# Kernel optimization log

Hardware: AMD Instinct MI355X
Metric: run time of the kernel (lower is better)

The kernel has to match this reference:

```python
import jax, jax.numpy as jnp
import numpy as np

B, M, P, A, T = 32, 128, 20, 32, 32
H = 32   # embed_size / local hidden
E = 64   # local_hidden_dim = 2*H, global attention embed dim


def setup_inputs() -> dict:
    key = jax.random.key(0)
    ks = jax.random.split(key, 10)
    def w(k, shape, fan):
        return jax.random.normal(k, shape, jnp.float32) / np.float32(np.sqrt(fan))
    z = lambda *s: jnp.zeros(s, jnp.float32)
    o = lambda *s: jnp.ones(s, jnp.float32)
    return {
        "map_states": jax.random.normal(ks[0], (B, M, P, 16), jnp.float32),
        "agent_states": jax.random.normal(ks[1], (B, A, T, 4), jnp.float32),
        "m_W1": w(ks[2], (16, H), 16), "m_b1": z(H), "m_g1": o(H), "m_be1": z(H),
        "m_W2": w(ks[3], (H, H), H),   "m_b2": z(H), "m_g2": o(H), "m_be2": z(H),
        "a_W1": w(ks[4], (4, H), 4),   "a_b1": z(H), "a_g1": o(H), "a_be1": z(H),
        "a_W2": w(ks[5], (H, H), H),   "a_b2": z(H), "a_g2": o(H), "a_be2": z(H),
        # stacked attention params: index 0 = a2m, 1 = agent(self), 2 = m2a
        "att_Wq": w(ks[6], (3, E, E), E), "att_bq": z(3, E),
        "att_Wk": w(ks[7], (3, E, E), E), "att_bk": z(3, E),
        "att_Wv": w(ks[8], (3, E, E), E), "att_bv": z(3, E),
        "att_Wo": w(ks[9], (3, E, E), E), "att_bo": z(3, E),
    }


def _mlp(x, W, b, g, be):
    # Linear -> LayerNorm -> ReLU
    h = x @ W + b
    mu = jnp.mean(h, axis=-1, keepdims=True)
    var = jnp.var(h, axis=-1, keepdims=True)
    h = (h - mu) / jnp.sqrt(var + 1e-5) * g + be
    return jax.nn.relu(h)


def _local_graph(x, p1, p2):
    # x: [B, N, P, F] -> [B, N, 2H]
    e = _mlp(_mlp(x, *p1), *p2)                       # [B,N,P,H]
    n = e.shape[2]
    # faithful "max excluding self": max_j (e[j] - 10000*[j==i])
    mask = -10000.0 * jnp.eye(n, dtype=e.dtype)       # [Pi,Pj]
    nb = jnp.max(e[:, :, None, :, :] + mask[None, None, :, :, None], axis=3)  # [B,N,P,H]
    e = jnp.concatenate([e, nb], axis=-1)             # [B,N,P,2H]
    return jnp.max(e, axis=2)                          # [B,N,2H]


def _mha(q, k, v, Wq, bq, Wk, bk, Wv, bv, Wo, bo):
    # single-head attention, batch_first
    d = q.shape[-1]
    Q = q @ Wq + bq
    K = k @ Wk + bk
    V = v @ Wv + bv
    scores = jnp.einsum('bqd,bkd->bqk', Q, K) / jnp.sqrt(jnp.asarray(d, Q.dtype))
    attn = jax.nn.softmax(scores, axis=-1)
    return jnp.einsum('bqk,bkd->bqd', attn, V) @ Wo + bo


def reference(map_states, agent_states,
              m_W1, m_b1, m_g1, m_be1, m_W2, m_b2, m_g2, m_be2,
              a_W1, a_b1, a_g1, a_be1, a_W2, a_b2, a_g2, a_be2,
              att_Wq, att_bq, att_Wk, att_bk, att_Wv, att_bv, att_Wo, att_bo):
    map_emb = _local_graph(map_states, (m_W1, m_b1, m_g1, m_be1), (m_W2, m_b2, m_g2, m_be2))      # [B,M,E]
    agent_emb = _local_graph(agent_states, (a_W1, a_b1, a_g1, a_be1), (a_W2, a_b2, a_g2, a_be2))  # [B,A,E]

    target = agent_emb[:, :1]                                       # [B,1,E]
    kv = jnp.concatenate([target, map_emb], axis=1)                 # [B,M+1,E]
    a2m = _mha(map_emb, kv, kv, att_Wq[0], att_bq[0], att_Wk[0], att_bk[0],
               att_Wv[0], att_bv[0], att_Wo[0], att_bo[0])
    map_emb = map_emb + a2m
    t_a = _mha(target, target, target, att_Wq[1], att_bq[1], att_Wk[1], att_bk[1],
               att_Wv[1], att_bv[1], att_Wo[1], att_bo[1])
    t_m2a = _mha(target, map_emb, map_emb, att_Wq[2], att_bq[2], att_Wk[2], att_bk[2],
                 att_Wv[2], att_bv[2], att_Wo[2], att_bo[2])
    target = t_a + t_m2a                                            # [B,1,E]
    # pack (target_agent_embedding, map_embedding) into one array [B, M+1, E]
    return jnp.concatenate([target, map_emb], axis=1)
```

## Files before the change

### kernel.cpp

```cpp
#include <hip/hip_runtime.h>

#define BB 32
#define MM 128
#define PP 20
#define AA 32
#define TT 32
#define HH 32
#define EE 64

__device__ __forceinline__ float4 matvec64(const float* __restrict__ W,
                                           const float* __restrict__ xrow,
                                           int s, int t)
{
    const float4* __restrict__ Wv = (const float4*)W;
    const float4* __restrict__ xv = (const float4*)xrow;
    float4 acc = make_float4(0.f, 0.f, 0.f, 0.f);
#pragma unroll
    for (int ii = 0; ii < 4; ++ii) {
        const float4 xx = xv[s * 4 + ii];
        const int ib = s * 16 + ii * 4;
        const float4 w0 = Wv[(ib + 0) * 16 + t];
        const float4 w1 = Wv[(ib + 1) * 16 + t];
        const float4 w2 = Wv[(ib + 2) * 16 + t];
        const float4 w3 = Wv[(ib + 3) * 16 + t];
        acc.x = fmaf(xx.x, w0.x, acc.x); acc.y = fmaf(xx.x, w0.y, acc.y);
        acc.z = fmaf(xx.x, w0.z, acc.z); acc.w = fmaf(xx.x, w0.w, acc.w);
        acc.x = fmaf(xx.y, w1.x, acc.x); acc.y = fmaf(xx.y, w1.y, acc.y);
        acc.z = fmaf(xx.y, w1.z, acc.z); acc.w = fmaf(xx.y, w1.w, acc.w);
        acc.x = fmaf(xx.z, w2.x, acc.x); acc.y = fmaf(xx.z, w2.y, acc.y);
        acc.z = fmaf(xx.z, w2.z, acc.z); acc.w = fmaf(xx.z, w2.w, acc.w);
        acc.x = fmaf(xx.w, w3.x, acc.x); acc.y = fmaf(xx.w, w3.y, acc.y);
        acc.z = fmaf(xx.w, w3.z, acc.z); acc.w = fmaf(xx.w, w3.w, acc.w);
    }
    acc.x += __shfl_xor(acc.x, 16); acc.y += __shfl_xor(acc.y, 16);
    acc.z += __shfl_xor(acc.z, 16); acc.w += __shfl_xor(acc.w, 16);
    acc.x += __shfl_xor(acc.x, 32); acc.y += __shfl_xor(acc.y, 32);
    acc.z += __shfl_xor(acc.z, 32); acc.w += __shfl_xor(acc.w, 32);
    return acc;
}

template <int IN>
__device__ __forceinline__ void lg_qkv_body(const float* __restrict__ xg, int P,
                                            const float* __restrict__ W1, const float* __restrict__ b1,
                                            const float* __restrict__ g1, const float* __restrict__ be1,
                                            const float* __restrict__ W2, const float* __restrict__ b2,
                                            const float* __restrict__ g2, const float* __restrict__ be2,
                                            float* __restrict__ embRow,
                                            const float* __restrict__ Wq, const float* __restrict__ bq,
                                            const float* __restrict__ Wk, const float* __restrict__ bk,
                                            const float* __restrict__ Wv, const float* __restrict__ bv,
                                            float* __restrict__ Qrow,
                                            float* __restrict__ Krow,
                                            float* __restrict__ Vrow)
{
    const int tid  = threadIdx.x;
    const int wave = tid >> 6;
    const int lane = tid & 63;
    const int sub  = tid >> 5;
    const int c    = tid & 31;

    __shared__ __align__(16) float aslot[4][32];
    __shared__ __align__(16) float wmax[2][32];
    __shared__ __align__(16) float xrow[EE];

    float w1c[IN];
#pragma unroll
    for (int k = 0; k < IN; ++k) w1c[k] = W1[k * HH + c];
    float w2c[HH];
#pragma unroll
    for (int k = 0; k < HH; ++k) w2c[k] = W2[k * HH + c];
    const float b1c = b1[c], g1c = g1[c], be1c = be1[c];
    const float b2c = b2[c], g2c = g2[c], be2c = be2[c];

    float cmax = -1e30f;

    for (int p0 = 0; p0 < P; p0 += 4) {
        const int p = p0 + sub;
        const float* xp = xg + (long)p * IN;

        float h = b1c;
        if (IN == 16) {
            const float4* xp4 = (const float4*)xp;
            const float4 x0 = xp4[0], x1 = xp4[1], x2 = xp4[2], x3 = xp4[3];
            h = fmaf(x0.x, w1c[0], h);  h = fmaf(x0.y, w1c[1], h);
            h = fmaf(x0.z, w1c[2], h);  h = fmaf(x0.w, w1c[3], h);
            h = fmaf(x1.x, w1c[4], h);  h = fmaf(x1.y, w1c[5], h);
            h = fmaf(x1.z, w1c[6], h);  h = fmaf(x1.w, w1c[7], h);
            h = fmaf(x2.x, w1c[8], h);  h = fmaf(x2.y, w1c[9], h);
            h = fmaf(x2.z, w1c[10], h); h = fmaf(x2.w, w1c[11], h);
            h = fmaf(x3.x, w1c[12], h); h = fmaf(x3.y, w1c[13], h);
            h = fmaf(x3.z, w1c[14], h); h = fmaf(x3.w, w1c[15], h);
        } else {
            const float4 x0 = *(const float4*)xp;
            h = fmaf(x0.x, w1c[0], h); h = fmaf(x0.y, w1c[1], h);
            h = fmaf(x0.z, w1c[2], h); h = fmaf(x0.w, w1c[3], h);
        }

        float sdot = h;
#pragma unroll
        for (int off = 16; off >= 1; off >>= 1) sdot += __shfl_xor(sdot, off, 32);
        const float mu = sdot * (1.0f / 32.0f);
        float d = h - mu;
        float sq = d * d;
#pragma unroll
        for (int off = 16; off >= 1; off >>= 1) sq += __shfl_xor(sq, off, 32);
        const float var = sq * (1.0f / 32.0f);
        float a = d * rsqrtf(var + 1e-5f) * g1c + be1c;
        a = fmaxf(a, 0.0f);

        aslot[sub][c] = a;
        const float4* av4 = (const float4*)aslot[sub];
        float h2 = b2c;
#pragma unroll
        for (int j = 0; j < 8; ++j) {
            const float4 aa = av4[j];
            h2 = fmaf(aa.x, w2c[4 * j + 0], h2);
            h2 = fmaf(aa.y, w2c[4 * j + 1], h2);
            h2 = fmaf(aa.z, w2c[4 * j + 2], h2);
            h2 = fmaf(aa.w, w2c[4 * j + 3], h2);
        }

        float s2 = h2;
#pragma unroll
        for (int off = 16; off >= 1; off >>= 1) s2 += __shfl_xor(s2, off, 32);
        const float mu2 = s2 * (1.0f / 32.0f);
        float d2 = h2 - mu2;
        float sq2 = d2 * d2;
#pragma unroll
        for (int off = 16; off >= 1; off >>= 1) sq2 += __shfl_xor(sq2, off, 32);
        const float var2 = sq2 * (1.0f / 32.0f);
        float e = d2 * rsqrtf(var2 + 1e-5f) * g2c + be2c;
        e = fmaxf(e, 0.0f);

        cmax = fmaxf(cmax, e);
    }

    cmax = fmaxf(cmax, __shfl_xor(cmax, 32));
    if (lane < 32) wmax[wave][lane] = cmax;
    __syncthreads();

    if (tid < 32) {
        const float fin = fmaxf(wmax[0][tid], wmax[1][tid]);
        xrow[tid]      = fin;
        xrow[tid + 32] = fin;
        embRow[tid]      = fin;
        embRow[tid + 32] = fin;
    }
    __syncthreads();

    const int s = lane >> 4, t = lane & 15;
    if (wave == 0) {
        if (Qrow) {
            float4 q4 = matvec64(Wq, xrow, s, t);
            if (s == 0) {
                const float4 bq4 = ((const float4*)bq)[t];
                float4 qo;
                qo.x = (q4.x + bq4.x) * 0.125f;
                qo.y = (q4.y + bq4.y) * 0.125f;
                qo.z = (q4.z + bq4.z) * 0.125f;
                qo.w = (q4.w + bq4.w) * 0.125f;
                ((float4*)Qrow)[t] = qo;
            }
        }
        float4 k4 = matvec64(Wk, xrow, s, t);
        if (s == 0) {
            const float4 kb4 = ((const float4*)bk)[t];
            float4 ko;
            ko.x = k4.x + kb4.x; ko.y = k4.y + kb4.y;
            ko.z = k4.z + kb4.z; ko.w = k4.w + kb4.w;
            ((float4*)Krow)[t] = ko;
        }
    } else {
        float4 v4 = matvec64(Wv, xrow, s, t);
        if (s == 0) {
            const float4 vb4 = ((const float4*)bv)[t];
            float4 vo;
            vo.x = v4.x + vb4.x; vo.y = v4.y + vb4.y;
            vo.z = v4.z + vb4.z; vo.w = v4.w + vb4.w;
            ((float4*)Vrow)[t] = vo;
        }
    }
}

__global__ void lg_qkv_kernel(const float* __restrict__ map_states,
                              const float* __restrict__ agent_states,
                              const float* __restrict__ mW1, const float* __restrict__ mb1,
                              const float* __restrict__ mg1, const float* __restrict__ mbe1,
                              const float* __restrict__ mW2, const float* __restrict__ mb2,
                              const float* __restrict__ mg2, const float* __restrict__ mbe2,
                              const float* __restrict__ aW1, const float* __restrict__ ab1,
                              const float* __restrict__ ag1, const float* __restrict__ abe1,
                              const float* __restrict__ aW2, const float* __restrict__ ab2,
                              const float* __restrict__ ag2, const float* __restrict__ abe2,
                              const float* __restrict__ Wq, const float* __restrict__ bq,
                              const float* __restrict__ Wk, const float* __restrict__ bk,
                              const float* __restrict__ Wv, const float* __restrict__ bv,
                              float* __restrict__ map_emb,
                              float* __restrict__ target,
                              float* __restrict__ Qb,
                              float* __restrict__ Kb,
                              float* __restrict__ Vb)
{
    const int g = blockIdx.x;
    if (g < BB * MM) {
        const int b = g >> 7, m = g & 127;
        lg_qkv_body<16>(map_states + (long)g * PP * 16, PP,
                        mW1, mb1, mg1, mbe1, mW2, mb2, mg2, mbe2,
                        map_emb + (long)g * EE,
                        Wq, bq, Wk, bk, Wv, bv,
                        Qb + (long)g * EE,
                        Kb + ((long)b * 129 + 1 + m) * EE,
                        Vb + ((long)b * 129 + 1 + m) * EE);
    } else {
        const int b = g - BB * MM;
        lg_qkv_body<4>(agent_states + (long)b * AA * TT * 4, TT,
                       aW1, ab1, ag1, abe1, aW2, ab2, ag2, abe2,
                       target + (long)b * EE,
                       Wq, bq, Wk, bk, Wv, bv,
                       nullptr,
                       Kb + (long)b * 129 * EE,
                       Vb + (long)b * 129 * EE);
    }
}

__global__ void attn_fused_kernel(const float* __restrict__ map_emb,
                                  const float* __restrict__ Qb,
                                  const float* __restrict__ Kb,
                                  const float* __restrict__ Vb,
                                  const float* __restrict__ Wo, const float* __restrict__ bo,
                                  const float* __restrict__ Wk2, const float* __restrict__ bk2,
                                  const float* __restrict__ Wv2, const float* __restrict__ bv2,
                                  float* __restrict__ K2,
                                  float* __restrict__ V2,
                                  float* __restrict__ out)
{
    const int blk  = blockIdx.x;
    const int b    = blk >> 7;
    const int q    = blk & 127;
    const int lane = threadIdx.x;
    const int s = lane >> 4, t = lane & 15;

    __shared__ __align__(16) float sc[132];
    __shared__ __align__(16) float av[EE];
    __shared__ __align__(16) float resrow[EE];

    const float4 q4 = ((const float4*)(Qb + ((long)b * MM + q) * EE))[t];

    const float* Kbase = Kb + (long)b * 129 * EE;
    float mx = -1e30f;
#pragma unroll 4
    for (int it = 0; it < 33; ++it) {
        const int j = it * 4 + s;
        const bool valid = (j < 129);
        float p = 0.0f;
        if (valid) {
            const float4 k4 = ((const float4*)(Kbase + (long)j * EE))[t];
            p = q4.x * k4.x + q4.y * k4.y + q4.z * k4.z + q4.w * k4.w;
        }
        p += __shfl_xor(p, 1); p += __shfl_xor(p, 2);
        p += __shfl_xor(p, 4); p += __shfl_xor(p, 8);
        if (valid) {
            mx = fmaxf(mx, p);
            if (t == 0) sc[j] = p;
        }
    }
#pragma unroll
    for (int off = 32; off >= 1; off >>= 1) mx = fmaxf(mx, __shfl_xor(mx, off));
    __syncthreads();

    float sum = 0.0f;
    for (int j = lane; j < 129; j += 64) {
        const float e = __expf(sc[j] - mx);
        sc[j] = e;
        sum += e;
    }
#pragma unroll
    for (int off = 32; off >= 1; off >>= 1) sum += __shfl_xor(sum, off);
    const float inv = 1.0f / sum;
    __syncthreads();

    const float* Vbase = Vb + (long)b * 129 * EE;
    float4 a4 = make_float4(0.f, 0.f, 0.f, 0.f);
#pragma unroll 4
    for (int it = 0; it < 33; ++it) {
        const int j = it * 4 + s;
        if (j < 129) {
            const float w = sc[j];
            const float4 v4 = ((const float4*)(Vbase + (long)j * EE))[t];
            a4.x = fmaf(w, v4.x, a4.x); a4.y = fmaf(w, v4.y, a4.y);
            a4.z = fmaf(w, v4.z, a4.z); a4.w = fmaf(w, v4.w, a4.w);
        }
    }
    a4.x += __shfl_xor(a4.x, 16); a4.y += __shfl_xor(a4.y, 16);
    a4.z += __shfl_xor(a4.z, 16); a4.w += __shfl_xor(a4.w, 16);
    a4.x += __shfl_xor(a4.x, 32); a4.y += __shfl_xor(a4.y, 32);
    a4.z += __shfl_xor(a4.z, 32); a4.w += __shfl_xor(a4.w, 32);
    if (s == 0) {
        float4 o; o.x = a4.x * inv; o.y = a4.y * inv; o.z = a4.z * inv; o.w = a4.w * inv;
        ((float4*)av)[t] = o;
    }
    __syncthreads();

    const float4 o4 = matvec64(Wo, av, s, t);
    const float4 bo4 = ((const float4*)bo)[t];
    const float4 x4 = ((const float4*)(map_emb + ((long)b * MM + q) * EE))[t];
    float4 res;
    res.x = o4.x + bo4.x + x4.x;
    res.y = o4.y + bo4.y + x4.y;
    res.z = o4.z + bo4.z + x4.z;
    res.w = o4.w + bo4.w + x4.w;
    if (s == 0) {
        ((float4*)(out + ((long)b * 129 + 1 + q) * EE))[t] = res;
        ((float4*)resrow)[t] = res;
    }
    __syncthreads();

    const float4 k4 = matvec64(Wk2, resrow, s, t);
    const float4 v4 = matvec64(Wv2, resrow, s, t);
    if (s == 0) {
        const float4 kb4 = ((const float4*)bk2)[t];
        const float4 vb4 = ((const float4*)bv2)[t];
        float4 ko, vo;
        ko.x = k4.x + kb4.x; ko.y = k4.y + kb4.y; ko.z = k4.z + kb4.z; ko.w = k4.w + kb4.w;
        vo.x = v4.x + vb4.x; vo.y = v4.y + vb4.y; vo.z = v4.z + vb4.z; vo.w = v4.w + vb4.w;
        ((float4*)(K2 + ((long)b * MM + q) * EE))[t] = ko;
        ((float4*)(V2 + ((long)b * MM + q) * EE))[t] = vo;
    }
}

__global__ void target_kernel(const float* __restrict__ target,
                              const float* __restrict__ K2, const float* __restrict__ V2,
                              const float* __restrict__ Wq2, const float* __restrict__ bq2,
                              const float* __restrict__ Wo2, const float* __restrict__ bo2,
                              const float* __restrict__ Wv1, const float* __restrict__ bv1,
                              const float* __restrict__ Wo1, const float* __restrict__ bo1,
                              float* __restrict__ out)
{
    const int b    = blockIdx.x;
    const int lane = threadIdx.x;
    const int s = lane >> 4, t = lane & 15;

    __shared__ __align__(16) float trow[EE];
    __shared__ __align__(16) float tmp[EE];
    __shared__ __align__(16) float sc[128];
    __shared__ __align__(16) float av[EE];

    trow[lane] = target[(long)b * EE + lane];
    __syncthreads();

    const float4 v1 = matvec64(Wv1, trow, s, t);
    if (s == 0) {
        const float4 bv4 = ((const float4*)bv1)[t];
        float4 w; w.x = v1.x + bv4.x; w.y = v1.y + bv4.y; w.z = v1.z + bv4.z; w.w = v1.w + bv4.w;
        ((float4*)tmp)[t] = w;
    }
    __syncthreads();
    float4 ta = matvec64(Wo1, tmp, s, t);
    {
        const float4 bo4 = ((const float4*)bo1)[t];
        ta.x += bo4.x; ta.y += bo4.y; ta.z += bo4.z; ta.w += bo4.w;
    }

    float4 q4 = matvec64(Wq2, trow, s, t);
    {
        const float4 bq4 = ((const float4*)bq2)[t];
        q4.x = (q4.x + bq4.x) * 0.125f;
        q4.y = (q4.y + bq4.y) * 0.125f;
        q4.z = (q4.z + bq4.z) * 0.125f;
        q4.w = (q4.w + bq4.w) * 0.125f;
    }

    const float* Kbase = K2 + (long)b * MM * EE;
    float mx = -1e30f;
#pragma unroll 4
    for (int it = 0; it < 32; ++it) {
        const int j = it * 4 + s;
        const float4 k4 = ((const float4*)(Kbase + (long)j * EE))[t];
        float p = q4.x * k4.x + q4.y * k4.y + q4.z * k4.z + q4.w * k4.w;
        p += __shfl_xor(p, 1); p += __shfl_xor(p, 2);
        p += __shfl_xor(p, 4); p += __shfl_xor(p, 8);
        mx = fmaxf(mx, p);
        if (t == 0) sc[j] = p;
    }
#pragma unroll
    for (int off = 32; off >= 1; off >>= 1) mx = fmaxf(mx, __shfl_xor(mx, off));
    __syncthreads();

    float sum = 0.0f;
#pragma unroll
    for (int j = lane; j < MM; j += 64) {
        const float e = __expf(sc[j] - mx);
        sc[j] = e;
        sum += e;
    }
#pragma unroll
    for (int off = 32; off >= 1; off >>= 1) sum += __shfl_xor(sum, off);
    const float inv = 1.0f / sum;
    __syncthreads();

    const float* Vbase = V2 + (long)b * MM * EE;
    float4 b4 = make_float4(0.f, 0.f, 0.f, 0.f);
#pragma unroll 4
    for (int it = 0; it < 32; ++it) {
        const int j = it * 4 + s;
        const float w = sc[j];
        const float4 vv = ((const float4*)(Vbase + (long)j * EE))[t];
        b4.x = fmaf(w, vv.x, b4.x); b4.y = fmaf(w, vv.y, b4.y);
        b4.z = fmaf(w, vv.z, b4.z); b4.w = fmaf(w, vv.w, b4.w);
    }
    b4.x += __shfl_xor(b4.x, 16); b4.y += __shfl_xor(b4.y, 16);
    b4.z += __shfl_xor(b4.z, 16); b4.w += __shfl_xor(b4.w, 16);
    b4.x += __shfl_xor(b4.x, 32); b4.y += __shfl_xor(b4.y, 32);
    b4.z += __shfl_xor(b4.z, 32); b4.w += __shfl_xor(b4.w, 32);
    if (s == 0) {
        float4 o; o.x = b4.x * inv; o.y = b4.y * inv; o.z = b4.z * inv; o.w = b4.w * inv;
        ((float4*)av)[t] = o;
    }
    __syncthreads();

    const float4 o4 = matvec64(Wo2, av, s, t);
    if (s == 0) {
        const float4 bo4 = ((const float4*)bo2)[t];
        float4 r;
        r.x = ta.x + o4.x + bo4.x;
        r.y = ta.y + o4.y + bo4.y;
        r.z = ta.z + o4.z + bo4.z;
        r.w = ta.w + o4.w + bo4.w;
        ((float4*)(out + (long)b * 129 * EE))[t] = r;
    }
}

extern "C" void kernel_launch(void* const* d_in, const int* in_sizes, int n_in,
                              void* d_out, int out_size, void* d_ws, size_t ws_size,
                              hipStream_t stream)
{
    const float* map_states   = (const float*)d_in[0];
    const float* agent_states = (const float*)d_in[1];
    const float* m_W1 = (const float*)d_in[2];
    const float* m_b1 = (const float*)d_in[3];
    const float* m_g1 = (const float*)d_in[4];
    const float* m_be1 = (const float*)d_in[5];
    const float* m_W2 = (const float*)d_in[6];
    const float* m_b2 = (const float*)d_in[7];
    const float* m_g2 = (const float*)d_in[8];
    const float* m_be2 = (const float*)d_in[9];
    const float* a_W1 = (const float*)d_in[10];
    const float* a_b1 = (const float*)d_in[11];
    const float* a_g1 = (const float*)d_in[12];
    const float* a_be1 = (const float*)d_in[13];
    const float* a_W2 = (const float*)d_in[14];
    const float* a_b2 = (const float*)d_in[15];
    const float* a_g2 = (const float*)d_in[16];
    const float* a_be2 = (const float*)d_in[17];
    const float* att_Wq = (const float*)d_in[18];
    const float* att_bq = (const float*)d_in[19];
    const float* att_Wk = (const float*)d_in[20];
    const float* att_bk = (const float*)d_in[21];
    const float* att_Wv = (const float*)d_in[22];
    const float* att_bv = (const float*)d_in[23];
    const float* att_Wo = (const float*)d_in[24];
    const float* att_bo = (const float*)d_in[25];

    float* out = (float*)d_out;

    float* ws      = (float*)d_ws;
    float* map_emb = ws;
    float* target  = map_emb + BB * MM * EE;
    float* Qb      = target + BB * EE;
    float* Kb      = Qb + BB * MM * EE;
    float* Vb      = Kb + BB * 129 * EE;
    float* K2      = Vb + BB * 129 * EE;
    float* V2      = K2 + BB * MM * EE;

    const float* Wq0 = att_Wq + 0 * EE * EE; const float* bq0 = att_bq + 0 * EE;
    const float* Wk0 = att_Wk + 0 * EE * EE; const float* bk0 = att_bk + 0 * EE;
    const float* Wv0 = att_Wv + 0 * EE * EE; const float* bv0 = att_bv + 0 * EE;
    const float* Wo0 = att_Wo + 0 * EE * EE; const float* bo0 = att_bo + 0 * EE;
    const float* Wv1 = att_Wv + 1 * EE * EE; const float* bv1 = att_bv + 1 * EE;
    const float* Wo1 = att_Wo + 1 * EE * EE; const float* bo1 = att_bo + 1 * EE;
    const float* Wq2 = att_Wq + 2 * EE * EE; const float* bq2 = att_bq + 2 * EE;
    const float* Wk2 = att_Wk + 2 * EE * EE; const float* bk2 = att_bk + 2 * EE;
    const float* Wv2 = att_Wv + 2 * EE * EE; const float* bv2 = att_bv + 2 * EE;
    const float* Wo2 = att_Wo + 2 * EE * EE; const float* bo2 = att_bo + 2 * EE;

    hipLaunchKernelGGL(lg_qkv_kernel, dim3(BB * MM + BB), dim3(128), 0, stream,
                       map_states, agent_states,
                       m_W1, m_b1, m_g1, m_be1, m_W2, m_b2, m_g2, m_be2,
                       a_W1, a_b1, a_g1, a_be1, a_W2, a_b2, a_g2, a_be2,
                       Wq0, bq0, Wk0, bk0, Wv0, bv0,
                       map_emb, target, Qb, Kb, Vb);

    hipLaunchKernelGGL(attn_fused_kernel, dim3(BB * MM), dim3(64), 0, stream,
                       map_emb, Qb, Kb, Vb, Wo0, bo0,
                       Wk2, bk2, Wv2, bv2, K2, V2, out);

    hipLaunchKernelGGL(target_kernel, dim3(BB), dim3(64), 0, stream,
                       target, K2, V2, Wq2, bq2, Wo2, bo2, Wv1, bv1, Wo1, bo1, out);
}
```

Before: 185.2 us.

## Widen local-graph blocks to 256 threads with preloaded inputs and one-pass LayerNorm

The local-graph kernel now runs 256 threads per block, so eight points are processed per pass instead of four, and all point inputs are loaded into registers up front with P as a compile-time constant. LayerNorm uses a single shuffle pass that reduces sum and sum of squares together, and the matvecs use split accumulators to shorten dependency chains. The Q, K and V projections are spread across three waves. The aim is fewer serial iterations and less reduction latency per block, at the cost of more registers, idle padded lanes when P=20, and slightly weaker numerical accuracy from the E[x²]-mu² variance formula.

```diff
diff --git a/kernel.cpp b/kernel.cpp
--- a/kernel.cpp
+++ b/kernel.cpp
@@ -39,8 +39,8 @@
     return acc;
 }
 
-template <int IN>
-__device__ __forceinline__ void lg_qkv_body(const float* __restrict__ xg, int P,
+template <int IN, int P>
+__device__ __forceinline__ void lg_qkv_body(const float* __restrict__ xg,
                                             const float* __restrict__ W1, const float* __restrict__ b1,
                                             const float* __restrict__ g1, const float* __restrict__ be1,
                                             const float* __restrict__ W2, const float* __restrict__ b2,
@@ -53,15 +53,26 @@
                                             float* __restrict__ Krow,
                                             float* __restrict__ Vrow)
 {
+    constexpr int NPASS = (P + 7) / 8;
     const int tid  = threadIdx.x;
     const int wave = tid >> 6;
     const int lane = tid & 63;
     const int sub  = tid >> 5;
     const int c    = tid & 31;
 
-    __shared__ __align__(16) float aslot[4][32];
-    __shared__ __align__(16) float wmax[2][32];
+    __shared__ __align__(16) float aslot[8][32];
+    __shared__ __align__(16) float wmax[4][32];
     __shared__ __align__(16) float xrow[EE];
+
+    float4 xr[NPASS][IN / 4];
+#pragma unroll
+    for (int ps = 0; ps < NPASS; ++ps) {
+        int p = ps * 8 + sub;
+        if (p > P - 1) p = P - 1;
+        const float4* xp4 = (const float4*)(xg + (long)p * IN);
+#pragma unroll
+        for (int j = 0; j < IN / 4; ++j) xr[ps][j] = xp4[j];
+    }
 
     float w1c[IN];
 #pragma unroll
@@ -74,65 +85,59 @@
 
     float cmax = -1e30f;
 
-    for (int p0 = 0; p0 < P; p0 += 4) {
-        const int p = p0 + sub;
-        const float* xp = xg + (long)p * IN;
-
-        float h = b1c;
-        if (IN == 16) {
-            const float4* xp4 = (const float4*)xp;
-            const float4 x0 = xp4[0], x1 = xp4[1], x2 = xp4[2], x3 = xp4[3];
-            h = fmaf(x0.x, w1c[0], h);  h = fmaf(x0.y, w1c[1], h);
-            h = fmaf(x0.z, w1c[2], h);  h = fmaf(x0.w, w1c[3], h);
-            h = fmaf(x1.x, w1c[4], h);  h = fmaf(x1.y, w1c[5], h);
-            h = fmaf(x1.z, w1c[6], h);  h = fmaf(x1.w, w1c[7], h);
-            h = fmaf(x2.x, w1c[8], h);  h = fmaf(x2.y, w1c[9], h);
-            h = fmaf(x2.z, w1c[10], h); h = fmaf(x2.w, w1c[11], h);
-            h = fmaf(x3.x, w1c[12], h); h = fmaf(x3.y, w1c[13], h);
-            h = fmaf(x3.z, w1c[14], h); h = fmaf(x3.w, w1c[15], h);
-        } else {
-            const float4 x0 = *(const float4*)xp;
-            h = fmaf(x0.x, w1c[0], h); h = fmaf(x0.y, w1c[1], h);
-            h = fmaf(x0.z, w1c[2], h); h = fmaf(x0.w, w1c[3], h);
-        }
-
-        float sdot = h;
-#pragma unroll
-        for (int off = 16; off >= 1; off >>= 1) sdot += __shfl_xor(sdot, off, 32);
-        const float mu = sdot * (1.0f / 32.0f);
-        float d = h - mu;
-        float sq = d * d;
-#pragma unroll
-        for (int off = 16; off >= 1; off >>= 1) sq += __shfl_xor(sq, off, 32);
-        const float var = sq * (1.0f / 32.0f);
-        float a = d * rsqrtf(var + 1e-5f) * g1c + be1c;
+#pragma unroll
+    for (int ps = 0; ps < NPASS; ++ps) {
+        const bool valid = (ps * 8 + sub) < P;
+
+        float ha = b1c, hb = 0.0f;
+#pragma unroll
+        for (int j = 0; j < IN / 4; ++j) {
+            const float4 xx = xr[ps][j];
+            ha = fmaf(xx.x, w1c[4 * j + 0], ha);
+            hb = fmaf(xx.y, w1c[4 * j + 1], hb);
+            ha = fmaf(xx.z, w1c[4 * j + 2], ha);
+            hb = fmaf(xx.w, w1c[4 * j + 3], hb);
+        }
+        const float h = ha + hb;
+
+        float s1 = h, s2 = h * h;
+#pragma unroll
+        for (int off = 16; off >= 1; off >>= 1) {
+            s1 += __shfl_xor(s1, off, 32);
+            s2 += __shfl_xor(s2, off, 32);
+        }
+        const float mu  = s1 * (1.0f / 32.0f);
+        float var = s2 * (1.0f / 32.0f) - mu * mu;
+        var = fmaxf(var, 0.0f);
+        float a = (h - mu) * rsqrtf(var + 1e-5f) * g1c + be1c;
         a = fmaxf(a, 0.0f);
 
         aslot[sub][c] = a;
         const float4* av4 = (const float4*)aslot[sub];
-        float h2 = b2c;
+        float h2a = b2c, h2b = 0.0f;
 #pragma unroll
         for (int j = 0; j < 8; ++j) {
             const float4 aa = av4[j];
-            h2 = fmaf(aa.x, w2c[4 * j + 0], h2);
-            h2 = fmaf(aa.y, w2c[4 * j + 1], h2);
-            h2 = fmaf(aa.z, w2c[4 * j + 2], h2);
-            h2 = fmaf(aa.w, w2c[4 * j + 3], h2);
-        }
-
-        float s2 = h2;
-#pragma unroll
-        for (int off = 16; off >= 1; off >>= 1) s2 += __shfl_xor(s2, off, 32);
-        const float mu2 = s2 * (1.0f / 32.0f);
-        float d2 = h2 - mu2;
-        float sq2 = d2 * d2;
-#pragma unroll
-        for (int off = 16; off >= 1; off >>= 1) sq2 += __shfl_xor(sq2, off, 32);
-        const float var2 = sq2 * (1.0f / 32.0f);
-        float e = d2 * rsqrtf(var2 + 1e-5f) * g2c + be2c;
+            h2a = fmaf(aa.x, w2c[4 * j + 0], h2a);
+            h2b = fmaf(aa.y, w2c[4 * j + 1], h2b);
+            h2a = fmaf(aa.z, w2c[4 * j + 2], h2a);
+            h2b = fmaf(aa.w, w2c[4 * j + 3], h2b);
+        }
+        const float h2 = h2a + h2b;
+
+        float t1 = h2, t2 = h2 * h2;
+#pragma unroll
+        for (int off = 16; off >= 1; off >>= 1) {
+            t1 += __shfl_xor(t1, off, 32);
+            t2 += __shfl_xor(t2, off, 32);
+        }
+        const float mu2  = t1 * (1.0f / 32.0f);
+        float var2 = t2 * (1.0f / 32.0f) - mu2 * mu2;
+        var2 = fmaxf(var2, 0.0f);
+        float e = (h2 - mu2) * rsqrtf(var2 + 1e-5f) * g2c + be2c;
         e = fmaxf(e, 0.0f);
 
-        cmax = fmaxf(cmax, e);
+        if (valid) cmax = fmaxf(cmax, e);
     }
 
     cmax = fmaxf(cmax, __shfl_xor(cmax, 32));
@@ -140,7 +145,8 @@
     __syncthreads();
 
     if (tid < 32) {
-        const float fin = fmaxf(wmax[0][tid], wmax[1][tid]);
+        float fin = fmaxf(fmaxf(wmax[0][tid], wmax[1][tid]),
+                          fmaxf(wmax[2][tid], wmax[3][tid]));
         xrow[tid]      = fin;
         xrow[tid + 32] = fin;
         embRow[tid]      = fin;
@@ -162,6 +168,7 @@
                 ((float4*)Qrow)[t] = qo;
             }
         }
+    } else if (wave == 1) {
         float4 k4 = matvec64(Wk, xrow, s, t);
         if (s == 0) {
             const float4 kb4 = ((const float4*)bk)[t];
@@ -170,7 +177,7 @@
             ko.z = k4.z + kb4.z; ko.w = k4.w + kb4.w;
             ((float4*)Krow)[t] = ko;
         }
-    } else {
+    } else if (wave == 2) {
         float4 v4 = matvec64(Wv, xrow, s, t);
         if (s == 0) {
             const float4 vb4 = ((const float4*)bv)[t];
@@ -182,7 +189,8 @@
     }
 }
 
-__global__ void lg_qkv_kernel(const float* __restrict__ map_states,
+__global__ __launch_bounds__(256) void lg_qkv_kernel(
+                              const float* __restrict__ map_states,
                               const float* __restrict__ agent_states,
                               const float* __restrict__ mW1, const float* __restrict__ mb1,
                               const float* __restrict__ mg1, const float* __restrict__ mbe1,
@@ -204,7 +212,7 @@
     const int g = blockIdx.x;
     if (g < BB * MM) {
         const int b = g >> 7, m = g & 127;
-        lg_qkv_body<16>(map_states + (long)g * PP * 16, PP,
+        lg_qkv_body<16, PP>(map_states + (long)g * PP * 16,
                         mW1, mb1, mg1, mbe1, mW2, mb2, mg2, mbe2,
                         map_emb + (long)g * EE,
                         Wq, bq, Wk, bk, Wv, bv,
@@ -213,7 +221,7 @@
                         Vb + ((long)b * 129 + 1 + m) * EE);
     } else {
         const int b = g - BB * MM;
-        lg_qkv_body<4>(agent_states + (long)b * AA * TT * 4, TT,
+        lg_qkv_body<4, TT>(agent_states + (long)b * AA * TT * 4,
                        aW1, ab1, ag1, abe1, aW2, ab2, ag2, abe2,
                        target + (long)b * EE,
                        Wq, bq, Wk, bk, Wv, bv,
@@ -483,7 +491,7 @@
     const float* Wv2 = att_Wv + 2 * EE * EE; const float* bv2 = att_bv + 2 * EE;
     const float* Wo2 = att_Wo + 2 * EE * EE; const float* bo2 = att_bo + 2 * EE;
 
-    hipLaunchKernelGGL(lg_qkv_kernel, dim3(BB * MM + BB), dim3(128), 0, stream,
+    hipLaunchKernelGGL(lg_qkv_kernel, dim3(BB * MM + BB), dim3(256), 0, stream,
                        map_states, agent_states,
                        m_W1, m_b1, m_g1, m_be1, m_W2, m_b2, m_g2, m_be2,
                        a_W1, a_b1, a_g1, a_be1, a_W2, a_b2, a_g2, a_be2,
```

After: 180.0 us. 1.03x faster.
